# Optimization experiments

Hardware: AMD Instinct MI355X
Metric: run time of the kernel (lower is better)

## Reference

```python
import jax, jax.numpy as jnp
import numpy as np

L = 4      # number of Verifier layers in the linked list
D = 1536   # constraint matrix dimension


def setup_inputs() -> dict:
    key = jax.random.key(0)
    ks = jax.random.split(key, 6)
    scale = 0.02  # keep chained matmul magnitudes sane
    lb = jax.random.normal(ks[0], (1, D), jnp.float32)
    ub = lb + jax.random.uniform(ks[1], (1, D), jnp.float32)  # ensure lb <= ub
    lcs = scale * jax.random.normal(ks[2], (L, D, D), jnp.float32)
    ucs = lcs + scale * jax.random.uniform(ks[3], (L, D, D), jnp.float32)
    lc_bias = jax.random.normal(ks[4], (L, D), jnp.float32)
    uc_bias = lc_bias + jax.random.uniform(ks[5], (L, D), jnp.float32)
    return {"lb": lb, "ub": ub, "lcs": lcs, "ucs": ucs,
            "lc_bias": lc_bias, "uc_bias": uc_bias}


def reference(lb, ub, lcs, ucs, lc_bias, uc_bias):
    pos = lambda x: jnp.maximum(x, 0.0)
    neg = lambda x: jnp.minimum(x, 0.0)
    n_layers = lcs.shape[0]

    # Layer 0 forward: its backsubstitution returns these bounds unchanged
    # (prev is None), and all later backsubs terminate on these stored bounds.
    lb0 = lb @ pos(lcs[0]).T + ub @ neg(lcs[0]).T + lc_bias[0]
    ub0 = ub @ pos(ucs[0]).T + lb @ neg(ucs[0]).T + uc_bias[0]
    cur_lb, cur_ub = lb0, ub0

    for k in range(1, n_layers):
        # backsubstitution from layer k: start with transposed constraint
        C_lc, C_uc = lcs[k].T, ucs[k].T           # [D, D]
        C_lcb, C_ucb = lc_bias[k], uc_bias[k]     # [D]
        # recurse through layers k-1 .. 0, combining constraints
        for j in range(k - 1, -1, -1):
            pU, nU = pos(C_uc), neg(C_uc)
            pL, nL = pos(C_lc), neg(C_lc)
            new_ucb = uc_bias[j] @ pU + lc_bias[j] @ nU + C_ucb
            new_uc = ucs[j].T @ pU + lcs[j].T @ nU
            new_lcb = lc_bias[j] @ pL + uc_bias[j] @ nL + C_lcb
            new_lc = lcs[j].T @ pL + ucs[j].T @ nL
            C_lc, C_uc, C_lcb, C_ucb = new_lc, new_uc, new_lcb, new_ucb
        # apply combined constraint to layer-0 stored bounds
        cur_lb = lb0 @ pos(C_lc) + ub0 @ neg(C_lc) + C_lcb
        cur_ub = ub0 @ pos(C_uc) + lb0 @ neg(C_uc) + C_ucb

    return cur_lb, cur_ub
```

## Files before the change

### kernel.cpp

```cpp
#include <hip/hip_runtime.h>

#define D 1536
#define BT 96
#define BK 64
#define NT (D / BK)
#define TT 64
#define TILE_E (BT * BK)
#define BUF_E (3 * TILE_E)

typedef unsigned short u16;
typedef short bf16x8 __attribute__((ext_vector_type(8)));
typedef float f32x4 __attribute__((ext_vector_type(4)));

static __device__ __forceinline__ u16 f2bf(float f) {
    unsigned u; __builtin_memcpy(&u, &f, 4);
    unsigned r = (u + 0x7FFFu + ((u >> 16) & 1u)) >> 16;
    return (u16)r;
}
static __device__ __forceinline__ float bf2f(u16 s) {
    unsigned u = ((unsigned)s) << 16;
    float f; __builtin_memcpy(&f, &u, 4); return f;
}

#define GLDS(g, s) __builtin_amdgcn_global_load_lds( \
    (const __attribute__((address_space(1))) void*)(g), \
    (__attribute__((address_space(3))) void*)(s), 16, 0, 0)

#define MFMA16(a, b, c) __builtin_amdgcn_mfma_f32_16x16x32_bf16(a, b, c, 0, 0, 0)

__global__ __launch_bounds__(256) void prep_k(
    const float* __restrict__ lcs, const float* __restrict__ ucs,
    u16* __restrict__ BsT, u16* __restrict__ BdT,
    u16* __restrict__ Ga, u16* __restrict__ Gc)
{
    const int z = blockIdx.z;
    const int r0 = blockIdx.y * TT, c0 = blockIdx.x * TT;
    const int tid = threadIdx.x;

    if (z == 3) {
#pragma unroll
        for (int m = 0; m < 2; ++m) {
            const float* src = (m ? lcs : ucs) + (size_t)3 * D * D;
            u16* dst = m ? Gc : Ga;
#pragma unroll
            for (int i = 0; i < 2; ++i) {
                int r = (tid >> 3) + i * 32, cc = (tid & 7) * 8;
                const float* p = src + (size_t)(r0 + r) * D + c0 + cc;
                f32x4 x0 = *(const f32x4*)p;
                f32x4 x1 = *(const f32x4*)(p + 4);
                bf16x8 y;
#pragma unroll
                for (int e = 0; e < 4; ++e) { y[e] = (short)f2bf(x0[e]); y[e + 4] = (short)f2bf(x1[e]); }
                *(bf16x8*)(dst + (size_t)(r0 + r) * D + c0 + cc) = y;
            }
        }
        return;
    }

    __shared__ u16 ts[TT][TT + 8];
    __shared__ u16 td[TT][TT + 8];
    const float* srcl = lcs + (size_t)z * D * D;
    const float* srcu = ucs + (size_t)z * D * D;
#pragma unroll
    for (int i = 0; i < 2; ++i) {
        int c = tid + i * 256; int r = c >> 3, v = c & 7;
        size_t off = (size_t)(r0 + r) * D + c0 + v * 8;
        f32x4 l0 = *(const f32x4*)(srcl + off);
        f32x4 l1 = *(const f32x4*)(srcl + off + 4);
        f32x4 u0 = *(const f32x4*)(srcu + off);
        f32x4 u1 = *(const f32x4*)(srcu + off + 4);
        bf16x8 ys, yd;
#pragma unroll
        for (int e = 0; e < 4; ++e) {
            ys[e]     = (short)f2bf((u0[e] + l0[e]) * 0.5f);
            yd[e]     = (short)f2bf((u0[e] - l0[e]) * 0.5f);
            ys[e + 4] = (short)f2bf((u1[e] + l1[e]) * 0.5f);
            yd[e + 4] = (short)f2bf((u1[e] - l1[e]) * 0.5f);
        }
        *(bf16x8*)&ts[r][v * 8] = ys;
        *(bf16x8*)&td[r][v * 8] = yd;
    }
    __syncthreads();
#pragma unroll
    for (int i = 0; i < 2; ++i) {
        int c = tid + i * 256; int rr = c >> 3, v = c & 7;
        bf16x8 xs, xd;
#pragma unroll
        for (int e = 0; e < 8; ++e) { xs[e] = (short)ts[v * 8 + e][rr]; xd[e] = (short)td[v * 8 + e][rr]; }
        size_t off = (size_t)z * D * D + (size_t)(c0 + rr) * D + r0 + v * 8;
        *(bf16x8*)(BsT + off) = xs;
        *(bf16x8*)(BdT + off) = xd;
    }
}

__global__ __launch_bounds__(256) void vec_k(
    const float* __restrict__ lb, const float* __restrict__ ub,
    const float* __restrict__ lcs, const float* __restrict__ ucs,
    const float* __restrict__ lcb, const float* __restrict__ ucb,
    float* __restrict__ lb0, float* __restrict__ ub0,
    float* __restrict__ cb_uc, float* __restrict__ cb_lc)
{
    const int tt = blockIdx.x * 4 + (threadIdx.x >> 6);
    const int lane = threadIdx.x & 63;
    const int which = tt / D;
    const int row_n = tt - which * D;

    const float* row; const float* vp; const float* vn;
    if (which == 0)      { row = lcs + (size_t)row_n * D;               vp = lb;           vn = ub; }
    else if (which == 1) { row = ucs + (size_t)row_n * D;               vp = ub;           vn = lb; }
    else if (which == 2) { row = ucs + (size_t)(3 * (size_t)D * D) + (size_t)row_n * D; vp = ucb + 2 * D; vn = lcb + 2 * D; }
    else                 { row = lcs + (size_t)(3 * (size_t)D * D) + (size_t)row_n * D; vp = lcb + 2 * D; vn = ucb + 2 * D; }

    float s = 0.f;
    for (int c2 = 0; c2 < D / 256; ++c2) {
        int base = (c2 * 64 + lane) * 4;
        f32x4 g = *(const f32x4*)(row + base);
        f32x4 p = *(const f32x4*)(vp + base);
        f32x4 m = *(const f32x4*)(vn + base);
#pragma unroll
        for (int e = 0; e < 4; ++e) s += g[e] * (g[e] > 0.f ? p[e] : m[e]);
    }
#pragma unroll
    for (int o = 32; o; o >>= 1) s += __shfl_down(s, o);
    if (lane == 0) {
        if (which == 0)      lb0[row_n] = s + lcb[row_n];
        else if (which == 1) ub0[row_n] = s + ucb[row_n];
        else if (which == 2) cb_uc[row_n] = s + ucb[3 * D + row_n];
        else                 cb_lc[row_n] = s + lcb[3 * D + row_n];
    }
}


static __device__ __forceinline__ void stage_tile(
    const u16* __restrict__ A, const u16* __restrict__ Bs, const u16* __restrict__ Bd,
    int r0, int c0, int kt, u16* __restrict__ sbuf, int tid, int wid)
{
#pragma unroll
    for (int i = 0; i < 9; ++i) {
        const int idx = (i % 3) * 256 + tid;
        const int row = idx >> 3;
        const int kcg = (tid & 7) ^ (row & 7);
        const u16* base = (i < 3) ? (A + (size_t)(r0 + row) * D)
                        : ((i < 6) ? (Bs + (size_t)(c0 + row) * D)
                                   : (Bd + (size_t)(c0 + row) * D));
        GLDS(base + kt + kcg * 8, (char*)sbuf + (i * 256 + wid * 64) * 16);
    }
}

static __device__ __forceinline__ void compute_tile(
    const u16* __restrict__ sbuf, f32x4 (&acc)[3][3], unsigned sgn,
    int mb, int nb, int lrow, int lk)
{
#pragma unroll
    for (int ks = 0; ks < 2; ++ks) {
        const int slot = ks * 4 + lk;
        bf16x8 a[3], x[3];
#pragma unroll
        for (int mi = 0; mi < 3; ++mi) {
            int row = mb + mi * 16 + lrow;
            int xx = slot ^ (row & 7);
            a[mi] = *(const bf16x8*)(sbuf + row * BK + xx * 8);
            union { bf16x8 v; unsigned u[4]; } t, o;
            t.v = a[mi];
#pragma unroll
            for (int q = 0; q < 4; ++q) o.u[q] = (t.u[q] & 0x7FFF7FFFu) ^ sgn;
            x[mi] = o.v;
        }
#pragma unroll
        for (int ni = 0; ni < 3; ++ni) {
            int row = nb + ni * 16 + lrow;
            int xx = slot ^ (row & 7);
            bf16x8 bs = *(const bf16x8*)(sbuf + TILE_E + row * BK + xx * 8);
            bf16x8 bd = *(const bf16x8*)(sbuf + 2 * TILE_E + row * BK + xx * 8);
#pragma unroll
            for (int mi = 0; mi < 3; ++mi) {
                acc[mi][ni] = MFMA16(a[mi], bs, acc[mi][ni]);
                acc[mi][ni] = MFMA16(x[mi], bd, acc[mi][ni]);
            }
        }
    }
}

__global__ __launch_bounds__(256, 2) void gemm_step(
    const u16* __restrict__ Guc, const u16* __restrict__ Glc,
    const u16* __restrict__ Bs, const u16* __restrict__ Bd,
    u16* __restrict__ outU, u16* __restrict__ outL,
    const float* __restrict__ ucbN, const float* __restrict__ lcbN,
    float* __restrict__ cb_uc, float* __restrict__ cb_lc)
{
    __shared__ u16 smem[2 * BUF_E];
    const int chain = blockIdx.z;
    const u16* A = chain ? Glc : Guc;
    u16* out = chain ? outL : outU;
    const unsigned sgn = chain ? 0x80008000u : 0u;
    const int r0 = blockIdx.y * BT, c0 = blockIdx.x * BT;
    const int tid = threadIdx.x, lane = tid & 63, wid = tid >> 6;
    const int mb = (wid >> 1) * 48, nb = (wid & 1) * 48;
    const int lrow = lane & 15, lk = lane >> 4;

    f32x4 acc[3][3] = {};

    stage_tile(A, Bs, Bd, r0, c0, 0, smem, tid, wid);
    stage_tile(A, Bs, Bd, r0, c0, BK, smem + BUF_E, tid, wid);

#pragma unroll 1
    for (int t = 0; t < NT; ++t) {
        if (t < NT - 1) { asm volatile("s_waitcnt vmcnt(9)" ::: "memory"); }
        else            { asm volatile("s_waitcnt vmcnt(0)" ::: "memory"); }
        __builtin_amdgcn_sched_barrier(0);
        __builtin_amdgcn_s_barrier();
        compute_tile(smem + (t & 1) * BUF_E, acc, sgn, mb, nb, lrow, lk);
        __builtin_amdgcn_s_barrier();
        if (t + 2 < NT)
            stage_tile(A, Bs, Bd, r0, c0, (t + 2) * BK, smem + (t & 1) * BUF_E, tid, wid);
    }

    if (ucbN) {
        const float* pb_ = chain ? lcbN : ucbN;
        const float* nb_ = chain ? ucbN : lcbN;
        float* cb = chain ? cb_lc : cb_uc;
        float pbv[3], nbv[3];
#pragma unroll
        for (int ni = 0; ni < 3; ++ni) {
            int c = c0 + nb + ni * 16 + lrow;
            pbv[ni] = pb_[c]; nbv[ni] = nb_[c];
        }
#pragma unroll
        for (int mi = 0; mi < 3; ++mi)
#pragma unroll
            for (int q = 0; q < 4; ++q) {
                float s = 0.f;
#pragma unroll
                for (int ni = 0; ni < 3; ++ni) {
                    float g = acc[mi][ni][q];
                    s += g * (g > 0.f ? pbv[ni] : nbv[ni]);
                }
                s += __shfl_xor(s, 1); s += __shfl_xor(s, 2);
                s += __shfl_xor(s, 4); s += __shfl_xor(s, 8);
                if (lrow == 0)
                    atomicAdd(&cb[r0 + mb + mi * 16 + lk * 4 + q], s);
            }
    }

#pragma unroll
    for (int mi = 0; mi < 3; ++mi)
#pragma unroll
        for (int ni = 0; ni < 3; ++ni) {
            int c = c0 + nb + ni * 16 + lrow;
            int rbase = r0 + mb + mi * 16 + lk * 4;
#pragma unroll
            for (int q = 0; q < 4; ++q)
                out[(size_t)(rbase + q) * D + c] = f2bf(acc[mi][ni][q]);
        }
}

__global__ __launch_bounds__(256) void final_k(
    const u16* __restrict__ Guc, const u16* __restrict__ Glc,
    const float* __restrict__ cb_uc, const float* __restrict__ cb_lc,
    const float* __restrict__ lb0, const float* __restrict__ ub0,
    float* __restrict__ out)
{
    const int gw = blockIdx.x * 4 + (threadIdx.x >> 6);
    const int lane = threadIdx.x & 63;
    const int which = gw >= D;
    const int n = which ? gw - D : gw;
    const u16* row = (which ? Guc : Glc) + (size_t)n * D;
    const float* vp = which ? ub0 : lb0;
    const float* vn = which ? lb0 : ub0;
    float s = 0.f;
    for (int c2 = 0; c2 < D / 512; ++c2) {
        int base = (c2 * 64 + lane) * 8;
        bf16x8 g8 = *(const bf16x8*)(row + base);
        f32x4 p0 = *(const f32x4*)(vp + base);
        f32x4 p1 = *(const f32x4*)(vp + base + 4);
        f32x4 n0 = *(const f32x4*)(vn + base);
        f32x4 n1 = *(const f32x4*)(vn + base + 4);
#pragma unroll
        for (int e = 0; e < 8; ++e) {
            float g = bf2f((u16)g8[e]);
            float pv = e < 4 ? p0[e] : p1[e - 4];
            float nv = e < 4 ? n0[e] : n1[e - 4];
            s += g * (g > 0.f ? pv : nv);
        }
    }
#pragma unroll
    for (int o = 32; o; o >>= 1) s += __shfl_down(s, o);
    if (lane == 0) {
        float b = (which ? cb_uc : cb_lc)[n];
        out[which * D + n] = s + b;
    }
}

extern "C" void kernel_launch(void* const* d_in, const int* in_sizes, int n_in,
                              void* d_out, int out_size, void* d_ws, size_t ws_size,
                              hipStream_t stream) {
    const float* lb  = (const float*)d_in[0];
    const float* ub  = (const float*)d_in[1];
    const float* lcs = (const float*)d_in[2];
    const float* ucs = (const float*)d_in[3];
    const float* lcb = (const float*)d_in[4];
    const float* ucb = (const float*)d_in[5];
    float* out = (float*)d_out;

    const size_t DD = (size_t)D * D;
    u16* ws   = (u16*)d_ws;
    u16* BsT = ws;
    u16* BdT = BsT + 3 * DD;
    u16* Ga = BdT + 3 * DD;
    u16* Gb = Ga + DD;
    u16* Gc = Gb + DD;
    u16* Gd = Gc + DD;
    float* fbuf  = (float*)(Gd + DD);
    float* lb0   = fbuf;
    float* ub0   = fbuf + D;
    float* cb_uc = fbuf + 2 * D;
    float* cb_lc = fbuf + 3 * D;

    prep_k<<<dim3(D / TT, D / TT, 4), 256, 0, stream>>>(lcs, ucs, BsT, BdT, Ga, Gc);
    vec_k<<<dim3(4 * D / 4), 256, 0, stream>>>(lb, ub, lcs, ucs, lcb, ucb, lb0, ub0, cb_uc, cb_lc);

    u16* curU = Ga; u16* curL = Gc;
    u16* altU = Gb; u16* altL = Gd;
    for (int j = 2; j >= 0; --j) {
        const float* ucbN = (j > 0) ? (ucb + (size_t)(j - 1) * D) : nullptr;
        const float* lcbN = (j > 0) ? (lcb + (size_t)(j - 1) * D) : nullptr;
        gemm_step<<<dim3(D / BT, D / BT, 2), 256, 0, stream>>>(
            curU, curL, BsT + (size_t)j * DD, BdT + (size_t)j * DD, altU, altL,
            ucbN, lcbN, cb_uc, cb_lc);
        u16* t;
        t = curU; curU = altU; altU = t;
        t = curL; curL = altL; altL = t;
    }
    final_k<<<dim3(2 * D / 4), 256, 0, stream>>>(curU, curL, cb_uc, cb_lc, lb0, ub0, out);
}
```

Before: 128.2 us.

## Halve K-tile and use 4-buffer LDS ring with single barrier per step

Reduces the K tile from 64 to 32 and switches from double-buffered LDS to a 4-slot ring, issuing the global-to-LDS loads for tile t+2 before computing tile t. This removes the second barrier per iteration. It also precomputes global pointers and LDS offsets, adopts a new swizzle suited to 32-wide rows, and raises wave priority around the MFMA block. The cost is twice as many loop iterations and barriers, uneven load counts per wave with per-wave vmcnt values, and a tighter dependence on those wait counts being exactly right.

Measured after the change: 188.2 us. 46.8% more time.

```diff
diff --git a/kernel.cpp b/kernel.cpp
--- a/kernel.cpp
+++ b/kernel.cpp
@@ -2,11 +2,12 @@
 
 #define D 1536
 #define BT 96
-#define BK 64
+#define BK 32
 #define NT (D / BK)
 #define TT 64
 #define TILE_E (BT * BK)
 #define BUF_E (3 * TILE_E)
+#define NCH (3 * BT * BK / 8)
 
 typedef unsigned short u16;
 typedef short bf16x8 __attribute__((ext_vector_type(8)));
@@ -130,57 +131,6 @@
     }
 }
 
-
-static __device__ __forceinline__ void stage_tile(
-    const u16* __restrict__ A, const u16* __restrict__ Bs, const u16* __restrict__ Bd,
-    int r0, int c0, int kt, u16* __restrict__ sbuf, int tid, int wid)
-{
-#pragma unroll
-    for (int i = 0; i < 9; ++i) {
-        const int idx = (i % 3) * 256 + tid;
-        const int row = idx >> 3;
-        const int kcg = (tid & 7) ^ (row & 7);
-        const u16* base = (i < 3) ? (A + (size_t)(r0 + row) * D)
-                        : ((i < 6) ? (Bs + (size_t)(c0 + row) * D)
-                                   : (Bd + (size_t)(c0 + row) * D));
-        GLDS(base + kt + kcg * 8, (char*)sbuf + (i * 256 + wid * 64) * 16);
-    }
-}
-
-static __device__ __forceinline__ void compute_tile(
-    const u16* __restrict__ sbuf, f32x4 (&acc)[3][3], unsigned sgn,
-    int mb, int nb, int lrow, int lk)
-{
-#pragma unroll
-    for (int ks = 0; ks < 2; ++ks) {
-        const int slot = ks * 4 + lk;
-        bf16x8 a[3], x[3];
-#pragma unroll
-        for (int mi = 0; mi < 3; ++mi) {
-            int row = mb + mi * 16 + lrow;
-            int xx = slot ^ (row & 7);
-            a[mi] = *(const bf16x8*)(sbuf + row * BK + xx * 8);
-            union { bf16x8 v; unsigned u[4]; } t, o;
-            t.v = a[mi];
-#pragma unroll
-            for (int q = 0; q < 4; ++q) o.u[q] = (t.u[q] & 0x7FFF7FFFu) ^ sgn;
-            x[mi] = o.v;
-        }
-#pragma unroll
-        for (int ni = 0; ni < 3; ++ni) {
-            int row = nb + ni * 16 + lrow;
-            int xx = slot ^ (row & 7);
-            bf16x8 bs = *(const bf16x8*)(sbuf + TILE_E + row * BK + xx * 8);
-            bf16x8 bd = *(const bf16x8*)(sbuf + 2 * TILE_E + row * BK + xx * 8);
-#pragma unroll
-            for (int mi = 0; mi < 3; ++mi) {
-                acc[mi][ni] = MFMA16(a[mi], bs, acc[mi][ni]);
-                acc[mi][ni] = MFMA16(x[mi], bd, acc[mi][ni]);
-            }
-        }
-    }
-}
-
 __global__ __launch_bounds__(256, 2) void gemm_step(
     const u16* __restrict__ Guc, const u16* __restrict__ Glc,
     const u16* __restrict__ Bs, const u16* __restrict__ Bd,
@@ -188,7 +138,7 @@
     const float* __restrict__ ucbN, const float* __restrict__ lcbN,
     float* __restrict__ cb_uc, float* __restrict__ cb_lc)
 {
-    __shared__ u16 smem[2 * BUF_E];
+    __shared__ u16 smem[4 * BUF_E];
     const int chain = blockIdx.z;
     const u16* A = chain ? Glc : Guc;
     u16* out = chain ? outL : outU;
@@ -198,21 +148,85 @@
     const int mb = (wid >> 1) * 48, nb = (wid & 1) * 48;
     const int lrow = lane & 15, lk = lane >> 4;
 
+    const int nld = (tid < 128) ? 5 : 4;
+    const u16* gp[5];
+    int ldso[5];
+#pragma unroll
+    for (int i = 0; i < 5; ++i) {
+        int c = tid + i * 256;
+        if (c < NCH) {
+            int b = c / 384, idx = c - b * 384;
+            int row = idx >> 2, kc = idx & 3;
+            int kcg = kc ^ ((row >> 1) & 3);
+            const u16* base = (b == 0) ? (A + (size_t)(r0 + row) * D)
+                            : ((b == 1) ? (Bs + (size_t)(c0 + row) * D)
+                                        : (Bd + (size_t)(c0 + row) * D));
+            gp[i] = base + kcg * 8;
+            ldso[i] = ((i * 256) + wid * 64) * 16;
+        } else { gp[i] = A; ldso[i] = 0; }
+    }
+
+    int offA[3], offBs[3], offBd[3];
+#pragma unroll
+    for (int mi = 0; mi < 3; ++mi) {
+        int row = mb + mi * 16 + lrow;
+        offA[mi] = row * BK + (lk ^ ((row >> 1) & 3)) * 8;
+    }
+#pragma unroll
+    for (int ni = 0; ni < 3; ++ni) {
+        int row = nb + ni * 16 + lrow;
+        int o = row * BK + (lk ^ ((row >> 1) & 3)) * 8;
+        offBs[ni] = TILE_E + o;
+        offBd[ni] = 2 * TILE_E + o;
+    }
+
     f32x4 acc[3][3] = {};
 
-    stage_tile(A, Bs, Bd, r0, c0, 0, smem, tid, wid);
-    stage_tile(A, Bs, Bd, r0, c0, BK, smem + BUF_E, tid, wid);
-
-#pragma unroll 1
+#pragma unroll
+    for (int t0 = 0; t0 < 2; ++t0)
+        for (int i = 0; i < nld; ++i)
+            GLDS(gp[i] + t0 * BK, (char*)smem + t0 * (BUF_E * 2) + ldso[i]);
+
+#pragma unroll 4
     for (int t = 0; t < NT; ++t) {
-        if (t < NT - 1) { asm volatile("s_waitcnt vmcnt(9)" ::: "memory"); }
-        else            { asm volatile("s_waitcnt vmcnt(0)" ::: "memory"); }
+        if (t + 2 < NT) {
+            const int tb = (t + 2) & 3;
+            for (int i = 0; i < nld; ++i)
+                GLDS(gp[i] + (t + 2) * BK, (char*)smem + tb * (BUF_E * 2) + ldso[i]);
+            if (wid < 2) { asm volatile("s_waitcnt vmcnt(10)" ::: "memory"); }
+            else         { asm volatile("s_waitcnt vmcnt(8)"  ::: "memory"); }
+        } else if (t + 2 == NT) {
+            if (wid < 2) { asm volatile("s_waitcnt vmcnt(5)" ::: "memory"); }
+            else         { asm volatile("s_waitcnt vmcnt(4)" ::: "memory"); }
+        } else {
+            asm volatile("s_waitcnt vmcnt(0)" ::: "memory");
+        }
         __builtin_amdgcn_sched_barrier(0);
         __builtin_amdgcn_s_barrier();
-        compute_tile(smem + (t & 1) * BUF_E, acc, sgn, mb, nb, lrow, lk);
-        __builtin_amdgcn_s_barrier();
-        if (t + 2 < NT)
-            stage_tile(A, Bs, Bd, r0, c0, (t + 2) * BK, smem + (t & 1) * BUF_E, tid, wid);
+
+        const u16* sb = smem + (t & 3) * BUF_E;
+        bf16x8 a[3], x[3];
+#pragma unroll
+        for (int mi = 0; mi < 3; ++mi) {
+            a[mi] = *(const bf16x8*)(sb + offA[mi]);
+            union { bf16x8 v; unsigned u[4]; } tt, oo;
+            tt.v = a[mi];
+#pragma unroll
+            for (int q = 0; q < 4; ++q) oo.u[q] = (tt.u[q] & 0x7FFF7FFFu) ^ sgn;
+            x[mi] = oo.v;
+        }
+        __builtin_amdgcn_s_setprio(1);
+#pragma unroll
+        for (int ni = 0; ni < 3; ++ni) {
+            bf16x8 bs = *(const bf16x8*)(sb + offBs[ni]);
+            bf16x8 bd = *(const bf16x8*)(sb + offBd[ni]);
+#pragma unroll
+            for (int mi = 0; mi < 3; ++mi) {
+                acc[mi][ni] = MFMA16(a[mi], bs, acc[mi][ni]);
+                acc[mi][ni] = MFMA16(x[mi], bd, acc[mi][ni]);
+            }
+        }
+        __builtin_amdgcn_s_setprio(0);
     }
 
     if (ucbN) {
```

## Load A operand directly into registers, stage only B tiles through LDS

Applied to the files above, without the earlier changes.

The GEMM step now reads the A operand straight from global memory into double-buffered registers, one K-tile ahead, instead of staging it through shared memory. Only the two B tiles are staged in LDS, which shrinks the shared buffer from three tiles to two per stage. The main loop is unrolled by two to alternate the register buffers, the vmcnt waits are retuned, and the MFMA block is wrapped in s_setprio. The aim is to cut LDS traffic and footprint and hide A-load latency. The cost is that the two waves sharing the same A rows now issue duplicate, less coalesced global loads and hold more registers.

Result: slower. 190.5 us (+48.6%).

```diff
diff --git a/kernel.cpp b/kernel.cpp
--- a/kernel.cpp
+++ b/kernel.cpp
@@ -6,7 +6,6 @@
 #define NT (D / BK)
 #define TT 64
 #define TILE_E (BT * BK)
-#define BUF_E (3 * TILE_E)
 
 typedef unsigned short u16;
 typedef short bf16x8 __attribute__((ext_vector_type(8)));
@@ -130,57 +129,6 @@
     }
 }
 
-
-static __device__ __forceinline__ void stage_tile(
-    const u16* __restrict__ A, const u16* __restrict__ Bs, const u16* __restrict__ Bd,
-    int r0, int c0, int kt, u16* __restrict__ sbuf, int tid, int wid)
-{
-#pragma unroll
-    for (int i = 0; i < 9; ++i) {
-        const int idx = (i % 3) * 256 + tid;
-        const int row = idx >> 3;
-        const int kcg = (tid & 7) ^ (row & 7);
-        const u16* base = (i < 3) ? (A + (size_t)(r0 + row) * D)
-                        : ((i < 6) ? (Bs + (size_t)(c0 + row) * D)
-                                   : (Bd + (size_t)(c0 + row) * D));
-        GLDS(base + kt + kcg * 8, (char*)sbuf + (i * 256 + wid * 64) * 16);
-    }
-}
-
-static __device__ __forceinline__ void compute_tile(
-    const u16* __restrict__ sbuf, f32x4 (&acc)[3][3], unsigned sgn,
-    int mb, int nb, int lrow, int lk)
-{
-#pragma unroll
-    for (int ks = 0; ks < 2; ++ks) {
-        const int slot = ks * 4 + lk;
-        bf16x8 a[3], x[3];
-#pragma unroll
-        for (int mi = 0; mi < 3; ++mi) {
-            int row = mb + mi * 16 + lrow;
-            int xx = slot ^ (row & 7);
-            a[mi] = *(const bf16x8*)(sbuf + row * BK + xx * 8);
-            union { bf16x8 v; unsigned u[4]; } t, o;
-            t.v = a[mi];
-#pragma unroll
-            for (int q = 0; q < 4; ++q) o.u[q] = (t.u[q] & 0x7FFF7FFFu) ^ sgn;
-            x[mi] = o.v;
-        }
-#pragma unroll
-        for (int ni = 0; ni < 3; ++ni) {
-            int row = nb + ni * 16 + lrow;
-            int xx = slot ^ (row & 7);
-            bf16x8 bs = *(const bf16x8*)(sbuf + TILE_E + row * BK + xx * 8);
-            bf16x8 bd = *(const bf16x8*)(sbuf + 2 * TILE_E + row * BK + xx * 8);
-#pragma unroll
-            for (int mi = 0; mi < 3; ++mi) {
-                acc[mi][ni] = MFMA16(a[mi], bs, acc[mi][ni]);
-                acc[mi][ni] = MFMA16(x[mi], bd, acc[mi][ni]);
-            }
-        }
-    }
-}
-
 __global__ __launch_bounds__(256, 2) void gemm_step(
     const u16* __restrict__ Guc, const u16* __restrict__ Glc,
     const u16* __restrict__ Bs, const u16* __restrict__ Bd,
@@ -188,7 +136,7 @@
     const float* __restrict__ ucbN, const float* __restrict__ lcbN,
     float* __restrict__ cb_uc, float* __restrict__ cb_lc)
 {
-    __shared__ u16 smem[2 * BUF_E];
+    __shared__ u16 smem[2 * 2 * TILE_E];
     const int chain = blockIdx.z;
     const u16* A = chain ? Glc : Guc;
     u16* out = chain ? outL : outU;
@@ -198,21 +146,82 @@
     const int mb = (wid >> 1) * 48, nb = (wid & 1) * 48;
     const int lrow = lane & 15, lk = lane >> 4;
 
+    const u16* Abase = A + (size_t)(r0 + mb + lrow) * D + lk * 8;
+
+    int offB[2][3];
+#pragma unroll
+    for (int ks = 0; ks < 2; ++ks)
+#pragma unroll
+        for (int ni = 0; ni < 3; ++ni) {
+            int row = nb + ni * 16 + lrow;
+            offB[ks][ni] = row * BK + ((ks * 4 + lk) ^ (row & 7)) * 8;
+        }
+
     f32x4 acc[3][3] = {};
-
-    stage_tile(A, Bs, Bd, r0, c0, 0, smem, tid, wid);
-    stage_tile(A, Bs, Bd, r0, c0, BK, smem + BUF_E, tid, wid);
+    bf16x8 Ae[3][2], Ao[3][2];
+
+#define LOAD_A(dst, t) do { \
+    _Pragma("unroll") for (int mi_ = 0; mi_ < 3; ++mi_) { \
+        const u16* ap_ = Abase + (size_t)(mi_ * 16) * D + (t) * BK; \
+        dst[mi_][0] = *(const bf16x8*)(ap_); \
+        dst[mi_][1] = *(const bf16x8*)(ap_ + 32); \
+    } } while (0)
+
+#define STAGE_B(kt, sbuf) do { \
+    _Pragma("unroll") for (int i_ = 0; i_ < 6; ++i_) { \
+        int c_ = tid + i_ * 256; \
+        int b_ = (i_ >= 3); \
+        int idx_ = c_ - b_ * 768; \
+        int row_ = idx_ >> 3, kc_ = idx_ & 7; \
+        int kcg_ = kc_ ^ (row_ & 7); \
+        const u16* base_ = (b_ ? Bd : Bs) + (size_t)(c0 + row_) * D + (kt) + kcg_ * 8; \
+        GLDS(base_, (char*)(sbuf) + (i_ * 256 + wid * 64) * 16); \
+    } } while (0)
+
+#define KSTEP(AREG, t) do { \
+    const u16* sb_ = smem + ((t) & 1) * (2 * TILE_E); \
+    bf16x8 xs_[3][2]; \
+    _Pragma("unroll") for (int mi_ = 0; mi_ < 3; ++mi_) \
+    _Pragma("unroll") for (int ks_ = 0; ks_ < 2; ++ks_) { \
+        union { bf16x8 v; unsigned u[4]; } ti_, to_; \
+        ti_.v = AREG[mi_][ks_]; \
+        _Pragma("unroll") for (int q_ = 0; q_ < 4; ++q_) to_.u[q_] = (ti_.u[q_] & 0x7FFF7FFFu) ^ sgn; \
+        xs_[mi_][ks_] = to_.v; } \
+    __builtin_amdgcn_s_setprio(1); \
+    _Pragma("unroll") for (int ks_ = 0; ks_ < 2; ++ks_) \
+    _Pragma("unroll") for (int ni_ = 0; ni_ < 3; ++ni_) { \
+        bf16x8 bs_ = *(const bf16x8*)(sb_ + offB[ks_][ni_]); \
+        bf16x8 bd_ = *(const bf16x8*)(sb_ + TILE_E + offB[ks_][ni_]); \
+        _Pragma("unroll") for (int mi_ = 0; mi_ < 3; ++mi_) { \
+            acc[mi_][ni_] = MFMA16(AREG[mi_][ks_], bs_, acc[mi_][ni_]); \
+            acc[mi_][ni_] = MFMA16(xs_[mi_][ks_], bd_, acc[mi_][ni_]); \
+        } } \
+    __builtin_amdgcn_s_setprio(0); \
+    } while (0)
+
+    STAGE_B(0, smem);
+    LOAD_A(Ae, 0);
+    STAGE_B(BK, smem + 2 * TILE_E);
 
 #pragma unroll 1
-    for (int t = 0; t < NT; ++t) {
-        if (t < NT - 1) { asm volatile("s_waitcnt vmcnt(9)" ::: "memory"); }
-        else            { asm volatile("s_waitcnt vmcnt(0)" ::: "memory"); }
+    for (int t2 = 0; t2 < NT / 2; ++t2) {
+        int t = 2 * t2;
+        LOAD_A(Ao, t + 1);
+        asm volatile("s_waitcnt vmcnt(12)" ::: "memory");
         __builtin_amdgcn_sched_barrier(0);
         __builtin_amdgcn_s_barrier();
-        compute_tile(smem + (t & 1) * BUF_E, acc, sgn, mb, nb, lrow, lk);
+        KSTEP(Ae, t);
         __builtin_amdgcn_s_barrier();
-        if (t + 2 < NT)
-            stage_tile(A, Bs, Bd, r0, c0, (t + 2) * BK, smem + (t & 1) * BUF_E, tid, wid);
+        if (t + 2 < NT) STAGE_B((t + 2) * BK, smem + (t & 1) * (2 * TILE_E));
+        ++t;
+        if (t + 1 < NT) LOAD_A(Ae, t + 1);
+        if (t < NT - 1) { asm volatile("s_waitcnt vmcnt(12)" ::: "memory"); }
+        else            { asm volatile("s_waitcnt vmcnt(0)"  ::: "memory"); }
+        __builtin_amdgcn_sched_barrier(0);
+        __builtin_amdgcn_s_barrier();
+        KSTEP(Ao, t);
+        __builtin_amdgcn_s_barrier();
+        if (t + 2 < NT) STAGE_B((t + 2) * BK, smem + (t & 1) * (2 * TILE_E));
     }
 
     if (ucbN) {
@@ -252,6 +261,9 @@
             for (int q = 0; q < 4; ++q)
                 out[(size_t)(rbase + q) * D + c] = f2bf(acc[mi][ni][q]);
         }
+#undef LOAD_A
+#undef STAGE_B
+#undef KSTEP
 }
 
 __global__ __launch_bounds__(256) void final_k(
```
